# Performance work log

Hardware: AMD Instinct MI355X
Metric: run time of the kernel (lower is better)

Reference implementation:

```python
import jax, jax.numpy as jnp
import numpy as np

N_NODES = 50000
N_EDGES = 600000
H_DIM = 128
BN_EPS = 1e-5


def setup_inputs() -> dict:
    key = jax.random.key(0)
    k1, k2, k3, k4 = jax.random.split(key, 4)
    ent_emb = jax.random.normal(k1, (N_NODES, H_DIM), dtype=jnp.float32)
    # xavier_normal_ init for the 128x128 weight
    std = float(np.sqrt(2.0 / (H_DIM + H_DIM)))
    neigh_w = jax.random.normal(k2, (H_DIM, H_DIM), dtype=jnp.float32) * std
    gamma = jnp.ones((H_DIM,), dtype=jnp.float32)
    beta = jnp.zeros((H_DIM,), dtype=jnp.float32)
    src = jax.random.randint(k3, (N_EDGES,), 0, N_NODES, dtype=jnp.int32)
    dst = jax.random.randint(k4, (N_EDGES,), 0, N_NODES, dtype=jnp.int32)
    return {"ent_emb": ent_emb, "neigh_w": neigh_w, "gamma": gamma,
            "beta": beta, "src": src, "dst": dst}


def reference(ent_emb, neigh_w, gamma, beta, src, dst):
    # Edge dot-product scores: u_dot_v('emb','emb')  -> [E]
    e_src = ent_emb[src]                      # [E, H]
    e_dst = ent_emb[dst]                      # [E, H]
    scores = jnp.sum(e_src * e_dst, axis=-1)  # [E]

    # edge_softmax: softmax over incoming edges of each destination node
    seg_max = jax.ops.segment_max(scores, dst, num_segments=N_NODES)
    seg_max = jnp.where(jnp.isfinite(seg_max), seg_max, 0.0)  # nodes w/o edges
    e = jnp.exp(scores - seg_max[dst])                         # [E]
    seg_sum = jax.ops.segment_sum(e, dst, num_segments=N_NODES)
    norm = e / seg_sum[dst]                                    # [E]

    # update_all(u_mul_e, sum): weighted gather-sum aggregation
    msg = e_src * norm[:, None]                                # [E, H]
    neigh = jax.ops.segment_sum(msg, dst, num_segments=N_NODES)  # [N, H]

    # matmul + BatchNorm1d (training-mode batch stats) + tanh
    h = neigh @ neigh_w                                        # [N, H]
    mean = jnp.mean(h, axis=0)
    var = jnp.var(h, axis=0)  # biased, matches torch BN normalization
    h = (h - mean) * jax.lax.rsqrt(var + BN_EPS) * gamma + beta
    return jnp.tanh(h)
```

## Files before the change

### kernel.cpp

```cpp
#include <hip/hip_runtime.h>
#include <math.h>

#define N_NODES 50000
#define N_EDGES 600000
#define H 128
#define BN_EPS 1e-5f
#define MAXDEG 48

__global__ void k_scatter(const int* __restrict__ src, const int* __restrict__ dst,
                          int* __restrict__ cnt, int* __restrict__ slots) {
    int i = blockIdx.x * blockDim.x + threadIdx.x;
    if (i < N_EDGES) {
        int d = dst[i];
        int pos = atomicAdd(cnt + d, 1);
        if (pos < MAXDEG) slots[d * MAXDEG + pos] = src[i];
    }
}

#define F4SCALE(a, s) { (a).x *= (s); (a).y *= (s); (a).z *= (s); (a).w *= (s); }
#define F4FMA(a, e, v) { (a).x += (e)*(v).x; (a).y += (e)*(v).y; (a).z += (e)*(v).z; (a).w += (e)*(v).w; }
#define F4SHFLADD(a, msk) { (a).x += __shfl_xor((a).x, msk, 64); (a).y += __shfl_xor((a).y, msk, 64); \
                            (a).z += __shfl_xor((a).z, msk, 64); (a).w += __shfl_xor((a).w, msk, 64); }

__global__ __launch_bounds__(256) void k_fused(const float* __restrict__ emb,
                                               const int* __restrict__ cnt,
                                               const int* __restrict__ slots,
                                               float* __restrict__ neigh) {
    int wid = (blockIdx.x * blockDim.x + threadIdx.x) >> 6;
    int lane = threadIdx.x & 63;
    if (wid >= N_NODES) return;
    int g = lane >> 3;
    int l = lane & 7;

    int deg = min(cnt[wid], MAXDEG);
    int sid = slots[wid * MAXDEG + min(lane, MAXDEG - 1)];

    const float4* rd = (const float4*)(emb + (size_t)wid * H) + l * 4;
    float4 b0 = rd[0], b1 = rd[1], b2 = rd[2], b3 = rd[3];

    float m = -INFINITY, ssum = 0.0f;
    float4 acc0 = {0,0,0,0}, acc1 = {0,0,0,0}, acc2 = {0,0,0,0}, acc3 = {0,0,0,0};

    for (int cb = 0; cb < deg; cb += 8) {
        int e = cb + g;
        bool valid = e < deg;
        int s = __shfl(sid, valid ? e : 0, 64);
        const float4* rs = (const float4*)(emb + (size_t)s * H) + l * 4;
        float4 a0 = rs[0], a1 = rs[1], a2 = rs[2], a3 = rs[3];

        float v = a0.x*b0.x + a0.y*b0.y + a0.z*b0.z + a0.w*b0.w
                + a1.x*b1.x + a1.y*b1.y + a1.z*b1.z + a1.w*b1.w
                + a2.x*b2.x + a2.y*b2.y + a2.z*b2.z + a2.w*b2.w
                + a3.x*b3.x + a3.y*b3.y + a3.z*b3.z + a3.w*b3.w;
        v += __shfl_xor(v, 1, 64);
        v += __shfl_xor(v, 2, 64);
        v += __shfl_xor(v, 4, 64);
        if (!valid) v = -INFINITY;

        float cmax = v;
        cmax = fmaxf(cmax, __shfl_xor(cmax, 8, 64));
        cmax = fmaxf(cmax, __shfl_xor(cmax, 16, 64));
        cmax = fmaxf(cmax, __shfl_xor(cmax, 32, 64));
        float mnew = fmaxf(m, cmax);
        float scale = __expf(m - mnew);
        ssum *= scale;
        F4SCALE(acc0, scale); F4SCALE(acc1, scale);
        F4SCALE(acc2, scale); F4SCALE(acc3, scale);
        m = mnew;

        float ev = __expf(v - m);
        ssum += ev;
        F4FMA(acc0, ev, a0); F4FMA(acc1, ev, a1);
        F4FMA(acc2, ev, a2); F4FMA(acc3, ev, a3);
    }

    ssum += __shfl_xor(ssum, 8, 64);
    ssum += __shfl_xor(ssum, 16, 64);
    ssum += __shfl_xor(ssum, 32, 64);
    F4SHFLADD(acc0, 8);  F4SHFLADD(acc1, 8);  F4SHFLADD(acc2, 8);  F4SHFLADD(acc3, 8);
    F4SHFLADD(acc0, 16); F4SHFLADD(acc1, 16); F4SHFLADD(acc2, 16); F4SHFLADD(acc3, 16);
    F4SHFLADD(acc0, 32); F4SHFLADD(acc1, 32); F4SHFLADD(acc2, 32); F4SHFLADD(acc3, 32);

    float inv = (deg > 0) ? 1.0f / ssum : 0.0f;
    if (g == 0) {
        float4* po = (float4*)(neigh + (size_t)wid * H) + l * 4;
        F4SCALE(acc0, inv); F4SCALE(acc1, inv); F4SCALE(acc2, inv); F4SCALE(acc3, inv);
        po[0] = acc0; po[1] = acc1; po[2] = acc2; po[3] = acc3;
    }
}

#define MM_ROWS 128
#define MM_COLS 64
__global__ __launch_bounds__(256, 4) void k_matmul(const float* __restrict__ neigh,
                                                   const float* __restrict__ W,
                                                   float* __restrict__ hout,
                                                   float* __restrict__ stats) {
    __shared__ float Wl[H * MM_COLS];
    __shared__ float Sl[16 * MM_COLS];
    __shared__ float Ql[16 * MM_COLS];
    int t = threadIdx.x;
    int bc = blockIdx.x & 1;
    int br = blockIdx.x >> 1;
    int c0 = bc * MM_COLS;
    int n0 = br * MM_ROWS;
    int cg = t & 15, rg = t >> 4;
    int j0 = cg * 4;
    int r0 = n0 + rg * 8;

    for (int idx = t; idx < H * 16; idx += 256) {
        int k = idx >> 4, c4 = idx & 15;
        *(float4*)&Wl[k * MM_COLS + c4 * 4] =
            *((const float4*)(W + (size_t)k * H + c0) + c4);
    }

    const float* pr[8];
    bool valid[8];
#pragma unroll
    for (int i = 0; i < 8; ++i) {
        int n = r0 + i;
        valid[i] = (n < N_NODES);
        pr[i] = neigh + (size_t)(valid[i] ? n : 0) * H;
    }

    __syncthreads();

    float acc[8][4] = {};
    for (int k0 = 0; k0 < H; k0 += 4) {
        float4 rv[8];
#pragma unroll
        for (int i = 0; i < 8; ++i) rv[i] = *(const float4*)(pr[i] + k0);
        float4 wv[4];
#pragma unroll
        for (int kk = 0; kk < 4; ++kk) wv[kk] = *(const float4*)&Wl[(k0 + kk) * MM_COLS + j0];
#pragma unroll
        for (int kk = 0; kk < 4; ++kk) {
#pragma unroll
            for (int i = 0; i < 8; ++i) {
                float rk = ((const float*)&rv[i])[kk];
                acc[i][0] += rk * wv[kk].x;
                acc[i][1] += rk * wv[kk].y;
                acc[i][2] += rk * wv[kk].z;
                acc[i][3] += rk * wv[kk].w;
            }
        }
    }

#pragma unroll
    for (int i = 0; i < 8; ++i) {
        if (valid[i]) {
            float4 o = make_float4(acc[i][0], acc[i][1], acc[i][2], acc[i][3]);
            *(float4*)(hout + (size_t)(r0 + i) * H + c0 + j0) = o;
        }
    }

#pragma unroll
    for (int c = 0; c < 4; ++c) {
        float s = 0.0f, q = 0.0f;
#pragma unroll
        for (int i = 0; i < 8; ++i) {
            if (valid[i]) { s += acc[i][c]; q += acc[i][c] * acc[i][c]; }
        }
        Sl[rg * MM_COLS + j0 + c] = s;
        Ql[rg * MM_COLS + j0 + c] = q;
    }
    __syncthreads();
    if (t < MM_COLS) {
        float s = 0.0f;
#pragma unroll
        for (int r = 0; r < 16; ++r) s += Sl[r * MM_COLS + t];
        atomicAdd(stats + c0 + t, s);
    } else if (t < 2 * MM_COLS) {
        int j = t - MM_COLS;
        float q = 0.0f;
#pragma unroll
        for (int r = 0; r < 16; ++r) q += Ql[r * MM_COLS + j];
        atomicAdd(stats + 128 + c0 + j, q);
    }
}

__device__ __forceinline__ float tanh_fast(float x) {
    float e = __expf(2.0f * x);
    return 1.0f - 2.0f / (e + 1.0f);
}

__global__ __launch_bounds__(256) void k_apply(float* __restrict__ h,
                                               const float* __restrict__ stats,
                                               const float* __restrict__ gamma,
                                               const float* __restrict__ beta) {
    __shared__ float sc[128], sh[128];
    int t = threadIdx.x;
    if (t < 128) {
        float mean = stats[t] * (1.0f / N_NODES);
        float var = stats[128 + t] * (1.0f / N_NODES) - mean * mean;
        var = fmaxf(var, 0.0f);
        float s = gamma[t] * rsqrtf(var + BN_EPS);
        sc[t] = s;
        sh[t] = beta[t] - mean * s;
    }
    __syncthreads();
    int i = blockIdx.x * 256 + t;
    if (i < N_NODES * H / 4) {
        float4 v = ((const float4*)h)[i];
        int jb = (i & 31) * 4;
        v.x = tanh_fast(v.x * sc[jb]     + sh[jb]);
        v.y = tanh_fast(v.y * sc[jb + 1] + sh[jb + 1]);
        v.z = tanh_fast(v.z * sc[jb + 2] + sh[jb + 2]);
        v.w = tanh_fast(v.w * sc[jb + 3] + sh[jb + 3]);
        ((float4*)h)[i] = v;
    }
}

extern "C" void kernel_launch(void* const* d_in, const int* in_sizes, int n_in,
                              void* d_out, int out_size, void* d_ws, size_t ws_size,
                              hipStream_t stream) {
    const float* emb   = (const float*)d_in[0];
    const float* W     = (const float*)d_in[1];
    const float* gamma = (const float*)d_in[2];
    const float* beta  = (const float*)d_in[3];
    const int*   src   = (const int*)d_in[4];
    const int*   dst   = (const int*)d_in[5];
    float* out = (float*)d_out;

    int*   cnt   = (int*)d_ws;
    float* stats = (float*)(cnt + N_NODES);
    int*   slots = (int*)(stats + 256);
    float* neigh = (float*)(slots + (size_t)N_NODES * MAXDEG);

    hipMemsetAsync(cnt, 0, (N_NODES + 256) * sizeof(int), stream);
    k_scatter<<<(N_EDGES + 255) / 256, 256, 0, stream>>>(src, dst, cnt, slots);
    k_fused<<<(N_NODES * 64 + 255) / 256, 256, 0, stream>>>(emb, cnt, slots, neigh);
    k_matmul<<<((N_NODES + MM_ROWS - 1) / MM_ROWS) * 2, 256, 0, stream>>>(neigh, W, out, stats);
    k_apply<<<(N_NODES * H / 4 + 255) / 256, 256, 0, stream>>>(out, stats, gamma, beta);
}
```

Before: 216.9 us.

## Vectorize edge scatter, split fused kernel in halves, prefetch matmul rows

Each scatter thread now handles two edges with int2 loads, halving the thread count. The fused aggregation kernel is launched twice, once per half of the nodes, on the same stream. The matmul inner loop software-prefetches the next k-slice of neigh rows into registers. Splitting the launch adds a launch boundary with no overlap, since both halves run on one stream, and the prefetch raises register pressure under launch_bounds(256,4).

```diff
diff --git a/kernel.cpp b/kernel.cpp
--- a/kernel.cpp
+++ b/kernel.cpp
@@ -6,11 +6,22 @@
 #define H 128
 #define BN_EPS 1e-5f
 #define MAXDEG 48
+#define MM_ROWS 128
+#define MM_COLS 64
+#define ROW_TILES ((N_NODES + MM_ROWS - 1) / MM_ROWS)
+#define N_TILES (ROW_TILES * 2)
 
 __global__ void k_scatter(const int* __restrict__ src, const int* __restrict__ dst,
                           int* __restrict__ cnt, int* __restrict__ slots) {
-    int i = blockIdx.x * blockDim.x + threadIdx.x;
-    if (i < N_EDGES) {
+    int i = (blockIdx.x * blockDim.x + threadIdx.x) * 2;
+    if (i + 1 < N_EDGES) {
+        int2 d2 = *(const int2*)(dst + i);
+        int2 s2 = *(const int2*)(src + i);
+        int p0 = atomicAdd(cnt + d2.x, 1);
+        int p1 = atomicAdd(cnt + d2.y, 1);
+        if (p0 < MAXDEG) slots[d2.x * MAXDEG + p0] = s2.x;
+        if (p1 < MAXDEG) slots[d2.y * MAXDEG + p1] = s2.y;
+    } else if (i < N_EDGES) {
         int d = dst[i];
         int pos = atomicAdd(cnt + d, 1);
         if (pos < MAXDEG) slots[d * MAXDEG + pos] = src[i];
@@ -25,10 +36,11 @@
 __global__ __launch_bounds__(256) void k_fused(const float* __restrict__ emb,
                                                const int* __restrict__ cnt,
                                                const int* __restrict__ slots,
-                                               float* __restrict__ neigh) {
-    int wid = (blockIdx.x * blockDim.x + threadIdx.x) >> 6;
+                                               float* __restrict__ neigh,
+                                               int n0, int n1) {
+    int wid = n0 + ((blockIdx.x * blockDim.x + threadIdx.x) >> 6);
     int lane = threadIdx.x & 63;
-    if (wid >= N_NODES) return;
+    if (wid >= n1) return;
     int g = lane >> 3;
     int l = lane & 7;
 
@@ -43,8 +55,8 @@
 
     for (int cb = 0; cb < deg; cb += 8) {
         int e = cb + g;
-        bool valid = e < deg;
-        int s = __shfl(sid, valid ? e : 0, 64);
+        bool ok = e < deg;
+        int s = __shfl(sid, ok ? e : 0, 64);
         const float4* rs = (const float4*)(emb + (size_t)s * H) + l * 4;
         float4 a0 = rs[0], a1 = rs[1], a2 = rs[2], a3 = rs[3];
 
@@ -55,7 +67,7 @@
         v += __shfl_xor(v, 1, 64);
         v += __shfl_xor(v, 2, 64);
         v += __shfl_xor(v, 4, 64);
-        if (!valid) v = -INFINITY;
+        if (!ok) v = -INFINITY;
 
         float cmax = v;
         cmax = fmaxf(cmax, __shfl_xor(cmax, 8, 64));
@@ -89,8 +101,6 @@
     }
 }
 
-#define MM_ROWS 128
-#define MM_COLS 64
 __global__ __launch_bounds__(256, 4) void k_matmul(const float* __restrict__ neigh,
                                                    const float* __restrict__ W,
                                                    float* __restrict__ hout,
@@ -103,8 +113,8 @@
     int br = blockIdx.x >> 1;
     int c0 = bc * MM_COLS;
     int n0 = br * MM_ROWS;
-    int cg = t & 15, rg = t >> 4;
-    int j0 = cg * 4;
+    int cg2 = t & 15, rg = t >> 4;
+    int j0 = cg2 * 4;
     int r0 = n0 + rg * 8;
 
     for (int idx = t; idx < H * 16; idx += 256) {
@@ -112,7 +122,6 @@
         *(float4*)&Wl[k * MM_COLS + c4 * 4] =
             *((const float4*)(W + (size_t)k * H + c0) + c4);
     }
-
     const float* pr[8];
     bool valid[8];
 #pragma unroll
@@ -121,14 +130,35 @@
         valid[i] = (n < N_NODES);
         pr[i] = neigh + (size_t)(valid[i] ? n : 0) * H;
     }
-
     __syncthreads();
 
     float acc[8][4] = {};
-    for (int k0 = 0; k0 < H; k0 += 4) {
-        float4 rv[8];
-#pragma unroll
-        for (int i = 0; i < 8; ++i) rv[i] = *(const float4*)(pr[i] + k0);
+    float4 rv[8], rvn[8];
+#pragma unroll
+    for (int i = 0; i < 8; ++i) rv[i] = *(const float4*)(pr[i]);
+
+    for (int k0 = 0; k0 < H - 4; k0 += 4) {
+#pragma unroll
+        for (int i = 0; i < 8; ++i) rvn[i] = *(const float4*)(pr[i] + k0 + 4);
+        float4 wv[4];
+#pragma unroll
+        for (int kk = 0; kk < 4; ++kk) wv[kk] = *(const float4*)&Wl[(k0 + kk) * MM_COLS + j0];
+#pragma unroll
+        for (int kk = 0; kk < 4; ++kk) {
+#pragma unroll
+            for (int i = 0; i < 8; ++i) {
+                float rk = ((const float*)&rv[i])[kk];
+                acc[i][0] += rk * wv[kk].x;
+                acc[i][1] += rk * wv[kk].y;
+                acc[i][2] += rk * wv[kk].z;
+                acc[i][3] += rk * wv[kk].w;
+            }
+        }
+#pragma unroll
+        for (int i = 0; i < 8; ++i) rv[i] = rvn[i];
+    }
+    {
+        int k0 = H - 4;
         float4 wv[4];
 #pragma unroll
         for (int kk = 0; kk < 4; ++kk) wv[kk] = *(const float4*)&Wl[(k0 + kk) * MM_COLS + j0];
@@ -191,8 +221,7 @@
     int t = threadIdx.x;
     if (t < 128) {
         float mean = stats[t] * (1.0f / N_NODES);
-        float var = stats[128 + t] * (1.0f / N_NODES) - mean * mean;
-        var = fmaxf(var, 0.0f);
+        float var = fmaxf(stats[128 + t] * (1.0f / N_NODES) - mean * mean, 0.0f);
         float s = gamma[t] * rsqrtf(var + BN_EPS);
         sc[t] = s;
         sh[t] = beta[t] - mean * s;
@@ -226,9 +255,12 @@
     int*   slots = (int*)(stats + 256);
     float* neigh = (float*)(slots + (size_t)N_NODES * MAXDEG);
 
+    const int NHALF = N_NODES / 2;
+
     hipMemsetAsync(cnt, 0, (N_NODES + 256) * sizeof(int), stream);
-    k_scatter<<<(N_EDGES + 255) / 256, 256, 0, stream>>>(src, dst, cnt, slots);
-    k_fused<<<(N_NODES * 64 + 255) / 256, 256, 0, stream>>>(emb, cnt, slots, neigh);
-    k_matmul<<<((N_NODES + MM_ROWS - 1) / MM_ROWS) * 2, 256, 0, stream>>>(neigh, W, out, stats);
+    k_scatter<<<(N_EDGES / 2 + 255) / 256, 256, 0, stream>>>(src, dst, cnt, slots);
+    k_fused<<<(NHALF * 64 + 255) / 256, 256, 0, stream>>>(emb, cnt, slots, neigh, 0, NHALF);
+    k_fused<<<((N_NODES - NHALF) * 64 + 255) / 256, 256, 0, stream>>>(emb, cnt, slots, neigh, NHALF, N_NODES);
+    k_matmul<<<N_TILES, 256, 0, stream>>>(neigh, W, out, stats);
     k_apply<<<(N_NODES * H / 4 + 255) / 256, 256, 0, stream>>>(out, stats, gamma, beta);
 }
```

Result: no change. 217.3 us (+0.2%).
